# Optimization experiments

Hardware: AMD Instinct MI355X
Metric: run time of the kernel (lower is better)

## Reference

```python
import jax, jax.numpy as jnp
import numpy as np

B, N, C, K, TOPK = 16, 4096, 256, 8, 2
EPS = 1e-6
RATIO = 0.1      # gate_geno_ratio
TEMP = 1.0       # gate_temperature


def setup_inputs() -> dict:
    key = jax.random.key(0)
    ks = jax.random.split(key, 8)
    s = np.float32(1.0 / np.sqrt(C))  # ~xavier scale for C->C linears
    return {
        "tokens": jax.random.normal(ks[0], (B, N, C), jnp.float32),
        "geno_vec": jax.random.normal(ks[1], (B, C), jnp.float32),
        # gate params (gate_proj init std=0.001; gate_geno given small random instead of exact-zero init so it contributes)
        "Wg": jax.random.normal(ks[2], (K, C), jnp.float32) * 0.001,
        "bg": jnp.zeros((K,), jnp.float32),
        "Wgg": jax.random.normal(ks[3], (K, C), jnp.float32) * 0.001,
        "bgg": jnp.zeros((K,), jnp.float32),
        # per-expert 2-layer MLP params (dropout inactive in eval)
        "W1": jax.random.normal(ks[4], (K, C, C), jnp.float32) * s,
        "b1": jnp.zeros((K, C), jnp.float32),
        "W2": jax.random.normal(ks[5], (K, C, C), jnp.float32) * s,
        "b2": jnp.zeros((K, C), jnp.float32),
    }


def reference(tokens, geno_vec, Wg, bg, Wgg, bgg, W1, b1, W2, b2):
    # gate logits: [B,N,K]
    logits = jnp.einsum("bnc,kc->bnk", tokens, Wg) + bg
    logits = logits + RATIO * (geno_vec @ Wgg.T + bgg)[:, None, :]
    logits = logits / TEMP

    topv, topi = jax.lax.top_k(logits, TOPK)          # [B,N,TOPK]
    topw = jax.nn.softmax(topv, axis=-1)
    topw = jnp.maximum(topw, EPS)
    topw = topw / topw.sum(-1, keepdims=True)

    # dense gate weight matrix W: [B,N,K] (scatter of topw at topi; topk indices are distinct)
    hot = jax.nn.one_hot(topi, K, dtype=tokens.dtype)  # [B,N,TOPK,K]
    Wmat = (hot * topw[..., None]).sum(-2)             # [B,N,K]

    # load-balance loss on hard usage (detached in original)
    usage = jax.lax.stop_gradient(hot.sum(-2).mean((0, 1)))  # [K]
    lb_loss = (jnp.std(usage) / (usage.mean() + EPS)) ** 2

    mass_sum = Wmat.sum(axis=1)                        # [B,K]

    # per-expert MLP computed densely over all tokens; zero gate weight kills
    # non-routed tokens exactly (same math as gather->MLP->scatter-add)
    def expert_center(k):
        h = jax.nn.relu(tokens @ W1[k].T + b1[k])      # [B,N,C]
        out = h @ W2[k].T + b2[k]                      # [B,N,C]
        return jnp.einsum("bn,bnc->bc", Wmat[:, :, k], out)

    centers_sum = jnp.stack([expert_center(k) for k in range(K)], axis=1)  # [B,K,C]
    centers = centers_sum / jnp.maximum(mass_sum, EPS)[..., None]

    routing_confidence = (topv[:, :, 0] - topv[:, :, 1]).mean()
    return centers, lb_loss, routing_confidence
```

## Files before the change

### kernel.cpp

```cpp
#include <hip/hip_runtime.h>

#define B_ 16
#define N_ 4096
#define C_ 256
#define K_ 8
#define EPS 1e-6f
#define RATIO 0.1f

typedef float f32x4 __attribute__((ext_vector_type(4)));
typedef __bf16 bf16x8 __attribute__((ext_vector_type(8)));

__device__ inline unsigned short f2bf(float f){
  unsigned int u = __float_as_uint(f);
  u += 0x7FFFu + ((u >> 16) & 1u);
  return (unsigned short)(u >> 16);
}
__device__ inline float bf2f(unsigned short h){
  return __uint_as_float(((unsigned int)h) << 16);
}

union BFu { ushort4 u4[2]; bf16x8 v; };

__global__ __launch_bounds__(256) void k0_prep(
    const float* __restrict__ W1, const float* __restrict__ Wg,
    const float* __restrict__ geno, const float* __restrict__ Wgg,
    const float* __restrict__ bgg,
    unsigned short* __restrict__ W1swz,
    unsigned short* __restrict__ Wgp_hi, unsigned short* __restrict__ Wgp_lo,
    int* __restrict__ cnt,
    float* __restrict__ mass, float* __restrict__ conf,
    float* __restrict__ glog)
{
  int gid = blockIdx.x * 256 + threadIdx.x;
  if (gid < B_*K_) { cnt[gid] = 0; mass[gid] = 0.f; }
  if (gid == 0) conf[0] = 0.f;
  {
    int o = gid << 3;
    int lane6 = (o >> 3) & 63;
    int s  = (o >> 9) & 7;
    int nt = (o >> 12) & 15;
    int k  = o >> 16;
    int quad = lane6 >> 4, l16 = lane6 & 15;
    int j  = nt*16 + l16;
    int c0 = s*32 + quad*8;
    const float* src = W1 + (k << 16) + (j << 8) + c0;
    unsigned short* dst = W1swz + o;
    #pragma unroll
    for (int e = 0; e < 8; ++e) dst[e] = f2bf(src[e]);
  }
  if (gid < 16*C_){
    int r = gid >> 8, c = gid & 255;
    float v = (r < K_) ? Wg[(r << 8) + c] : 0.f;
    unsigned short h = f2bf(v);
    Wgp_hi[gid] = h;
    Wgp_lo[gid] = f2bf(v - bf2f(h));
  }
  int wv = gid >> 6;
  if (wv < B_*K_){
    int lane = threadIdx.x & 63;
    int b = wv >> 3, k = wv & 7;
    float4 a = *(const float4*)(geno + b*C_ + lane*4);
    float4 w = *(const float4*)(Wgg  + k*C_ + lane*4);
    float p = a.x*w.x + a.y*w.y + a.z*w.z + a.w*w.w;
    #pragma unroll
    for (int off = 32; off; off >>= 1) p += __shfl_xor(p, off);
    if (lane == 0) glog[wv] = RATIO * (p + bgg[k]);
  }
}

__global__ __launch_bounds__(256) void k1_gate(
    const float* __restrict__ tokens,
    const unsigned short* __restrict__ Wgp_hi, const unsigned short* __restrict__ Wgp_lo,
    const float* __restrict__ bg, const float* __restrict__ glog,
    int* __restrict__ cnt, int* __restrict__ bidx, float* __restrict__ bw,
    float* __restrict__ mass, float* __restrict__ conf,
    unsigned short* __restrict__ tok_bf)
{
  __shared__ float ls[64][9];
  __shared__ float bg_s[K_], gl_s[K_], mass_s[K_];
  __shared__ int lcnt[K_], gbase[K_];
  __shared__ int e0s[64], e1s[64], s0s[64], s1s[64];
  __shared__ float w0s[64], w1s[64];
  int tid = threadIdx.x, lane = tid & 63, wave = tid >> 6;
  int quad = lane >> 4, l16 = lane & 15;
  int b = blockIdx.x >> 6;
  int tok0 = (blockIdx.x & 63) * 64;
  if (tid < K_){ bg_s[tid] = bg[tid]; gl_s[tid] = glog[b*K_ + tid];
                 mass_s[tid] = 0.f; lcnt[tid] = 0; }
  __syncthreads();

  {
    int trow = tok0 + wave*16 + l16;
    const float* xsrc = tokens + ((size_t)b*N_ + trow)*C_ + quad*8;
    unsigned short* bdst = tok_bf + (((size_t)(b*N_ + trow)) << 8) + quad*8;
    f32x4 acc; acc.x = 0.f; acc.y = 0.f; acc.z = 0.f; acc.w = 0.f;
    #pragma unroll
    for (int s = 0; s < 8; ++s){
      float4 xa = *(const float4*)(xsrc + s*32);
      float4 xb = *(const float4*)(xsrc + s*32 + 4);
      BFu hi, lo;
      hi.u4[0].x = f2bf(xa.x); hi.u4[0].y = f2bf(xa.y);
      hi.u4[0].z = f2bf(xa.z); hi.u4[0].w = f2bf(xa.w);
      hi.u4[1].x = f2bf(xb.x); hi.u4[1].y = f2bf(xb.y);
      hi.u4[1].z = f2bf(xb.z); hi.u4[1].w = f2bf(xb.w);
      lo.u4[0].x = f2bf(xa.x - bf2f(hi.u4[0].x));
      lo.u4[0].y = f2bf(xa.y - bf2f(hi.u4[0].y));
      lo.u4[0].z = f2bf(xa.z - bf2f(hi.u4[0].z));
      lo.u4[0].w = f2bf(xa.w - bf2f(hi.u4[0].w));
      lo.u4[1].x = f2bf(xb.x - bf2f(hi.u4[1].x));
      lo.u4[1].y = f2bf(xb.y - bf2f(hi.u4[1].y));
      lo.u4[1].z = f2bf(xb.z - bf2f(hi.u4[1].z));
      lo.u4[1].w = f2bf(xb.w - bf2f(hi.u4[1].w));
      *(ushort4*)(bdst + s*32)     = hi.u4[0];
      *(ushort4*)(bdst + s*32 + 4) = hi.u4[1];
      bf16x8 bhi = *(const bf16x8*)(Wgp_hi + l16*C_ + s*32 + quad*8);
      bf16x8 blo = *(const bf16x8*)(Wgp_lo + l16*C_ + s*32 + quad*8);
      acc = __builtin_amdgcn_mfma_f32_16x16x32_bf16(hi.v, bhi, acc, 0, 0, 0);
      acc = __builtin_amdgcn_mfma_f32_16x16x32_bf16(lo.v, bhi, acc, 0, 0, 0);
      acc = __builtin_amdgcn_mfma_f32_16x16x32_bf16(hi.v, blo, acc, 0, 0, 0);
    }
    if (l16 < K_){
      #pragma unroll
      for (int rr = 0; rr < 4; ++rr){
        int tl = wave*16 + quad*4 + rr;
        ls[tl][l16] = acc[rr] + bg_s[l16] + gl_s[l16];
      }
    }
  }
  __syncthreads();

  if (tid < 64){
    int t = tid;
    float v0 = -1e30f, v1 = -1e30f; int i0 = 0, i1 = 0;
    #pragma unroll
    for (int kk = 0; kk < K_; ++kk){
      float l = ls[t][kk];
      if (l > v0){ v1 = v0; i1 = i0; v0 = l; i0 = kk; }
      else if (l > v1){ v1 = l; i1 = kk; }
    }
    float e  = expf(v1 - v0);
    float w0 = 1.f / (1.f + e), w1 = e / (1.f + e);
    w0 = fmaxf(w0, EPS); w1 = fmaxf(w1, EPS);
    float inv = 1.f / (w0 + w1);
    w0 *= inv; w1 *= inv;
    int p0 = atomicAdd(&lcnt[i0], 1);
    int p1 = atomicAdd(&lcnt[i1], 1);
    e0s[t] = i0; e1s[t] = i1; s0s[t] = p0; s1s[t] = p1;
    w0s[t] = w0; w1s[t] = w1;
    atomicAdd(&mass_s[i0], w0);
    atomicAdd(&mass_s[i1], w1);
    float ca = v0 - v1;
    #pragma unroll
    for (int off = 32; off; off >>= 1) ca += __shfl_down(ca, off);
    if (t == 0) atomicAdd(conf, ca);
  }
  __syncthreads();
  if (tid < K_){
    gbase[tid] = atomicAdd(&cnt[b*K_ + tid], lcnt[tid]);
    atomicAdd(&mass[b*K_ + tid], mass_s[tid]);
  }
  __syncthreads();
  if (tid < 64){
    int t = tid;
    int n = tok0 + t;
    int ke0 = e0s[t], ke1 = e1s[t];
    size_t o0 = (size_t)(b*K_ + ke0)*N_ + gbase[ke0] + s0s[t];
    size_t o1 = (size_t)(b*K_ + ke1)*N_ + gbase[ke1] + s1s[t];
    bidx[o0] = n;  bw[o0] = w0s[t];
    bidx[o1] = n;  bw[o1] = w1s[t];
  }
}

__global__ void k2_scalars(const int* __restrict__ cnt, const float* __restrict__ conf,
                           float* __restrict__ out)
{
  __shared__ int kc[K_];
  int tid = threadIdx.x;
  if (tid < K_) kc[tid] = 0;
  __syncthreads();
  if (tid < B_*K_) atomicAdd(&kc[tid & 7], cnt[tid]);
  __syncthreads();
  if (tid == 0){
    float u[K_], mean = 0.f;
    for (int k = 0; k < K_; ++k){ u[k] = (float)kc[k] / (float)(B_*N_); mean += u[k]; }
    mean *= (1.f / K_);
    float var = 0.f;
    for (int k = 0; k < K_; ++k){ float d = u[k] - mean; var += d*d; }
    var *= (1.f / K_);
    float denom = mean + EPS;
    out[B_*K_*C_]     = var / (denom * denom);
    out[B_*K_*C_ + 1] = conf[0] / (float)(B_*N_);
  }
}

__global__ __launch_bounds__(256, 4) void k4_expert(
    const unsigned short* __restrict__ tok_bf, const unsigned short* __restrict__ W1swz,
    const float* __restrict__ b1, const int* __restrict__ cnt,
    const int* __restrict__ bidx, const float* __restrict__ bw,
    float* __restrict__ gpart)
{
  int lin = blockIdx.x;
  int w = (lin & 7) * 512 + (lin >> 3);
  int bat = w >> 8;
  int k = (w >> 5) & 7;
  int chunk = w & 31;
  int bucket = (bat << 3) | k;
  int M = cnt[bucket];
  if (chunk * 128 >= M) return;
  int Mm1 = M - 1;

  __shared__ unsigned short Bs[16384];
  __shared__ float wtok[128];
  __shared__ float red[4][64];

  int tid = threadIdx.x, lane = tid & 63, wave = tid >> 6;
  int quad = lane >> 4, l16 = lane & 15;
  int bwbase = bucket << 12;

  const unsigned short* wsrc = W1swz + ((size_t)k << 16);
  #pragma unroll
  for (int i = 0; i < 8; ++i){
    int c16 = i*256 + tid;
    __builtin_amdgcn_global_load_lds(
      (const __attribute__((address_space(1))) unsigned int*)(wsrc + c16*8),
      (__attribute__((address_space(3))) unsigned int*)(Bs + c16*8), 16, 0, 0);
  }

  if (tid < 128){
    int tn = chunk*128 + tid;
    wtok[tid] = (tn < M) ? bw[bwbase + tn] : 0.f;
  }

  int r0 = chunk*128 + (wave << 4) + l16;
  int r1 = r0 + 64;
  int nn0 = bidx[bwbase + min(r0, Mm1)];
  int nn1 = bidx[bwbase + min(r1, Mm1)];
  const unsigned short* p0 = tok_bf + (((size_t)((bat << 12) + nn0)) << 8) + (quad << 3);
  const unsigned short* p1 = tok_bf + (((size_t)((bat << 12) + nn1)) << 8) + (quad << 3);
  bf16x8 a0[8], a1[8];
  #pragma unroll
  for (int s = 0; s < 8; ++s){
    a0[s] = *(const bf16x8*)(p0 + s*32);
    a1[s] = *(const bf16x8*)(p1 + s*32);
  }

  #pragma unroll 1
  for (int jt = 0; jt < 4; ++jt){
    __syncthreads();

    f32x4 acc[2][4];
    #pragma unroll
    for (int mt = 0; mt < 2; ++mt)
      #pragma unroll
      for (int t = 0; t < 4; ++t){ acc[mt][t].x=0.f; acc[mt][t].y=0.f; acc[mt][t].z=0.f; acc[mt][t].w=0.f; }
    #pragma unroll
    for (int s = 0; s < 8; ++s){
      #pragma unroll
      for (int t = 0; t < 4; ++t){
        bf16x8 bb = *(const bf16x8*)(Bs + (((t*8 + s)*64 + lane) << 3));
        acc[0][t] = __builtin_amdgcn_mfma_f32_16x16x32_bf16(a0[s], bb, acc[0][t], 0,0,0);
        acc[1][t] = __builtin_amdgcn_mfma_f32_16x16x32_bf16(a1[s], bb, acc[1][t], 0,0,0);
      }
    }
    #pragma unroll
    for (int t = 0; t < 4; ++t){
      float bias = b1[(k << 8) + (jt << 6) + (t << 4) + l16];
      float pt = 0.f;
      #pragma unroll
      for (int mt = 0; mt < 2; ++mt){
        #pragma unroll
        for (int rr = 0; rr < 4; ++rr){
          float h = fmaxf(acc[mt][t][rr] + bias, 0.f);
          pt += wtok[mt*64 + (wave << 4) + (quad << 2) + rr] * h;
        }
      }
      pt += __shfl_down(pt, 32);
      pt += __shfl_down(pt, 16);
      if (lane < 16) red[wave][(t << 4) + lane] = pt;
    }
    __syncthreads();
    if (tid < 64){
      float sv = red[0][tid] + red[1][tid] + red[2][tid] + red[3][tid];
      gpart[(size_t)((((bucket << 5) + chunk) << 8) + (jt << 6) + tid)] = sv;
    }
    if (jt < 3){
      const unsigned short* ws2 = wsrc + ((jt + 1) << 14);
      #pragma unroll
      for (int i = 0; i < 8; ++i){
        int c16 = i*256 + tid;
        __builtin_amdgcn_global_load_lds(
          (const __attribute__((address_space(1))) unsigned int*)(ws2 + c16*8),
          (__attribute__((address_space(3))) unsigned int*)(Bs + c16*8), 16, 0, 0);
      }
    }
  }
}

__global__ __launch_bounds__(256) void k5_centers(
    const float* __restrict__ gpart, const int* __restrict__ cnt,
    const float* __restrict__ W2, const float* __restrict__ b2,
    const float* __restrict__ mass, float* __restrict__ out)
{
  __shared__ float gv[C_];
  int z = blockIdx.x, tid = threadIdx.x;
  int k = z & 7;
  int nch = (cnt[z] + 127) >> 7;
  float sv = 0.f;
  for (int c = 0; c < nch; ++c)
    sv += gpart[(size_t)((((z << 5) + c) << 8) + tid)];
  gv[tid] = sv;
  __syncthreads();
  float m = mass[z];
  float inv = 1.f / fmaxf(m, EPS);
  int tq = tid & 3, cb = tid >> 2;
  #pragma unroll 1
  for (int h = 0; h < 2; ++h){
    int c = (blockIdx.y*2 + h)*64 + cb;
    const float4* wrow = (const float4*)(W2 + ((((k << 8) + c)) << 8));
    float dot = 0.f;
    #pragma unroll
    for (int jj = 0; jj < 16; ++jj){
      float4 w4 = wrow[jj*4 + tq];
      float4 g4 = *(const float4*)&gv[(jj*4 + tq) * 4];
      dot += w4.x*g4.x + w4.y*g4.y + w4.z*g4.z + w4.w*g4.w;
    }
    dot += __shfl_xor(dot, 1);
    dot += __shfl_xor(dot, 2);
    if (tq == 0) out[z*C_ + c] = (dot + m * b2[k*C_ + c]) * inv;
  }
}

extern "C" void kernel_launch(void* const* d_in, const int* in_sizes, int n_in,
                              void* d_out, int out_size, void* d_ws, size_t ws_size,
                              hipStream_t stream)
{
  const float* tokens = (const float*)d_in[0];
  const float* geno   = (const float*)d_in[1];
  const float* Wg     = (const float*)d_in[2];
  const float* bg     = (const float*)d_in[3];
  const float* Wgg    = (const float*)d_in[4];
  const float* bgg    = (const float*)d_in[5];
  const float* W1     = (const float*)d_in[6];
  const float* b1     = (const float*)d_in[7];
  const float* W2     = (const float*)d_in[8];
  const float* b2     = (const float*)d_in[9];
  float* out = (float*)d_out;
  char* ws = (char*)d_ws;
  unsigned short* W1swz  = (unsigned short*)(ws);
  unsigned short* Wgp_hi = (unsigned short*)(ws + 1048576);
  unsigned short* Wgp_lo = (unsigned short*)(ws + 1056768);
  float* glog = (float*)(ws + 1196032);
  int*   cnt  = (int*)  (ws + 1196544);
  float* mass = (float*)(ws + 1197056);
  float* conf = (float*)(ws + 1197568);
  int*   bidx = (int*)  (ws + 1198080);
  float* bw   = (float*)(ws + 3295232);
  unsigned short* tok_bf = (unsigned short*)(ws + 5392384);
  float* gpart = (float*)(ws + 38946816);

  k0_prep<<<256, 256, 0, stream>>>(W1, Wg, geno, Wgg, bgg, W1swz, Wgp_hi, Wgp_lo,
                                   cnt, mass, conf, glog);
  k1_gate<<<1024, 256, 0, stream>>>(tokens, Wgp_hi, Wgp_lo, bg, glog,
                                    cnt, bidx, bw, mass, conf, tok_bf);
  k2_scalars<<<1, 128, 0, stream>>>(cnt, conf, out);
  k4_expert<<<4096, 256, 0, stream>>>(tok_bf, W1swz, b1, cnt, bidx, bw, gpart);
  k5_centers<<<dim3(128, 2), 256, 0, stream>>>(gpart, cnt, W2, b2, mass, out);
}
```

Measured before the change: 184.0 us.

## Pipeline W1 tiles through a 4-slot LDS ring in expert kernel; fold scalars into k5

```diff
diff --git a/kernel.cpp b/kernel.cpp
--- a/kernel.cpp
+++ b/kernel.cpp
@@ -171,28 +171,6 @@
   }
 }
 
-__global__ void k2_scalars(const int* __restrict__ cnt, const float* __restrict__ conf,
-                           float* __restrict__ out)
-{
-  __shared__ int kc[K_];
-  int tid = threadIdx.x;
-  if (tid < K_) kc[tid] = 0;
-  __syncthreads();
-  if (tid < B_*K_) atomicAdd(&kc[tid & 7], cnt[tid]);
-  __syncthreads();
-  if (tid == 0){
-    float u[K_], mean = 0.f;
-    for (int k = 0; k < K_; ++k){ u[k] = (float)kc[k] / (float)(B_*N_); mean += u[k]; }
-    mean *= (1.f / K_);
-    float var = 0.f;
-    for (int k = 0; k < K_; ++k){ float d = u[k] - mean; var += d*d; }
-    var *= (1.f / K_);
-    float denom = mean + EPS;
-    out[B_*K_*C_]     = var / (denom * denom);
-    out[B_*K_*C_ + 1] = conf[0] / (float)(B_*N_);
-  }
-}
-
 __global__ __launch_bounds__(256, 4) void k4_expert(
     const unsigned short* __restrict__ tok_bf, const unsigned short* __restrict__ W1swz,
     const float* __restrict__ b1, const int* __restrict__ cnt,
@@ -209,21 +187,26 @@
   if (chunk * 128 >= M) return;
   int Mm1 = M - 1;
 
-  __shared__ unsigned short Bs[16384];
+  __shared__ unsigned short Bs[4][4096];
   __shared__ float wtok[128];
-  __shared__ float red[4][64];
+  __shared__ float red[2][4][16];
 
   int tid = threadIdx.x, lane = tid & 63, wave = tid >> 6;
   int quad = lane >> 4, l16 = lane & 15;
   int bwbase = bucket << 12;
 
   const unsigned short* wsrc = W1swz + ((size_t)k << 16);
+
   #pragma unroll
-  for (int i = 0; i < 8; ++i){
-    int c16 = i*256 + tid;
-    __builtin_amdgcn_global_load_lds(
-      (const __attribute__((address_space(1))) unsigned int*)(wsrc + c16*8),
-      (__attribute__((address_space(3))) unsigned int*)(Bs + c16*8), 16, 0, 0);
+  for (int pp = 0; pp < 2; ++pp){
+    #pragma unroll
+    for (int i = 0; i < 2; ++i){
+      int c16 = pp*512 + i*256 + tid;
+      __builtin_amdgcn_global_load_lds(
+        (const __attribute__((address_space(1))) unsigned int*)(wsrc + c16*8),
+        (__attribute__((address_space(3))) unsigned int*)(&Bs[pp][0] + (i*256 + tid)*8),
+        16, 0, 0);
+    }
   }
 
   if (tid < 128){
@@ -232,9 +215,8 @@
   }
 
   int r0 = chunk*128 + (wave << 4) + l16;
-  int r1 = r0 + 64;
   int nn0 = bidx[bwbase + min(r0, Mm1)];
-  int nn1 = bidx[bwbase + min(r1, Mm1)];
+  int nn1 = bidx[bwbase + min(r0 + 64, Mm1)];
   const unsigned short* p0 = tok_bf + (((size_t)((bat << 12) + nn0)) << 8) + (quad << 3);
   const unsigned short* p1 = tok_bf + (((size_t)((bat << 12) + nn1)) << 8) + (quad << 3);
   bf16x8 a0[8], a1[8];
@@ -244,62 +226,72 @@
     a1[s] = *(const bf16x8*)(p1 + s*32);
   }
 
-  #pragma unroll 1
-  for (int jt = 0; jt < 4; ++jt){
-    __syncthreads();
-
-    f32x4 acc[2][4];
-    #pragma unroll
-    for (int mt = 0; mt < 2; ++mt)
+  float bias[16];
+  #pragma unroll
+  for (int p = 0; p < 16; ++p) bias[p] = b1[(k << 8) + (p << 4) + l16];
+
+  float* gdst = gpart + (size_t)(((bucket << 5) + chunk) << 8);
+  int wq = (wave << 4) + (quad << 2);
+
+  #pragma unroll
+  for (int p = 0; p < 16; ++p){
+    if (p < 14){
       #pragma unroll
-      for (int t = 0; t < 4; ++t){ acc[mt][t].x=0.f; acc[mt][t].y=0.f; acc[mt][t].z=0.f; acc[mt][t].w=0.f; }
+      for (int i = 0; i < 2; ++i){
+        int c16 = (p + 2)*512 + i*256 + tid;
+        __builtin_amdgcn_global_load_lds(
+          (const __attribute__((address_space(1))) unsigned int*)(wsrc + c16*8),
+          (__attribute__((address_space(3))) unsigned int*)(&Bs[(p + 2) & 3][0] + (i*256 + tid)*8),
+          16, 0, 0);
+      }
+      asm volatile("s_waitcnt vmcnt(4) lgkmcnt(0)" ::: "memory");
+    } else if (p == 14){
+      asm volatile("s_waitcnt vmcnt(2) lgkmcnt(0)" ::: "memory");
+    } else {
+      asm volatile("s_waitcnt vmcnt(0) lgkmcnt(0)" ::: "memory");
+    }
+    __builtin_amdgcn_s_barrier();
+
+    if (p > 0 && tid < 16){
+      int pb = (p - 1) & 1;
+      float sv = red[pb][0][tid] + red[pb][1][tid]
+               + red[pb][2][tid] + red[pb][3][tid];
+      gdst[((p - 1) << 4) + tid] = sv;
+    }
+
+    f32x4 acc0, acc1;
+    acc0.x=0.f; acc0.y=0.f; acc0.z=0.f; acc0.w=0.f;
+    acc1.x=0.f; acc1.y=0.f; acc1.z=0.f; acc1.w=0.f;
     #pragma unroll
     for (int s = 0; s < 8; ++s){
-      #pragma unroll
-      for (int t = 0; t < 4; ++t){
-        bf16x8 bb = *(const bf16x8*)(Bs + (((t*8 + s)*64 + lane) << 3));
-        acc[0][t] = __builtin_amdgcn_mfma_f32_16x16x32_bf16(a0[s], bb, acc[0][t], 0,0,0);
-        acc[1][t] = __builtin_amdgcn_mfma_f32_16x16x32_bf16(a1[s], bb, acc[1][t], 0,0,0);
-      }
-    }
-    #pragma unroll
-    for (int t = 0; t < 4; ++t){
-      float bias = b1[(k << 8) + (jt << 6) + (t << 4) + l16];
-      float pt = 0.f;
-      #pragma unroll
-      for (int mt = 0; mt < 2; ++mt){
-        #pragma unroll
-        for (int rr = 0; rr < 4; ++rr){
-          float h = fmaxf(acc[mt][t][rr] + bias, 0.f);
-          pt += wtok[mt*64 + (wave << 4) + (quad << 2) + rr] * h;
-        }
-      }
-      pt += __shfl_down(pt, 32);
-      pt += __shfl_down(pt, 16);
-      if (lane < 16) red[wave][(t << 4) + lane] = pt;
-    }
-    __syncthreads();
-    if (tid < 64){
-      float sv = red[0][tid] + red[1][tid] + red[2][tid] + red[3][tid];
-      gpart[(size_t)((((bucket << 5) + chunk) << 8) + (jt << 6) + tid)] = sv;
-    }
-    if (jt < 3){
-      const unsigned short* ws2 = wsrc + ((jt + 1) << 14);
-      #pragma unroll
-      for (int i = 0; i < 8; ++i){
-        int c16 = i*256 + tid;
-        __builtin_amdgcn_global_load_lds(
-          (const __attribute__((address_space(1))) unsigned int*)(ws2 + c16*8),
-          (__attribute__((address_space(3))) unsigned int*)(Bs + c16*8), 16, 0, 0);
-      }
-    }
+      bf16x8 bb = *(const bf16x8*)(&Bs[p & 3][0] + ((s*64 + lane) << 3));
+      acc0 = __builtin_amdgcn_mfma_f32_16x16x32_bf16(a0[s], bb, acc0, 0, 0, 0);
+      acc1 = __builtin_amdgcn_mfma_f32_16x16x32_bf16(a1[s], bb, acc1, 0, 0, 0);
+    }
+    float pt = 0.f;
+    #pragma unroll
+    for (int rr = 0; rr < 4; ++rr){
+      float h0 = fmaxf(acc0[rr] + bias[p], 0.f);
+      float h1 = fmaxf(acc1[rr] + bias[p], 0.f);
+      pt += wtok[wq + rr] * h0 + wtok[64 + wq + rr] * h1;
+    }
+    pt += __shfl_down(pt, 32);
+    pt += __shfl_down(pt, 16);
+    if (lane < 16) red[p & 1][wave][lane] = pt;
+  }
+  asm volatile("s_waitcnt lgkmcnt(0)" ::: "memory");
+  __builtin_amdgcn_s_barrier();
+  if (tid < 16){
+    float sv = red[1][0][tid] + red[1][1][tid] + red[1][2][tid] + red[1][3][tid];
+    gdst[(15 << 4) + tid] = sv;
   }
 }
 
 __global__ __launch_bounds__(256) void k5_centers(
     const float* __restrict__ gpart, const int* __restrict__ cnt,
     const float* __restrict__ W2, const float* __restrict__ b2,
-    const float* __restrict__ mass, float* __restrict__ out)
+    const float* __restrict__ mass, const float* __restrict__ conf,
+    float* __restrict__ out)
 {
   __shared__ float gv[C_];
   int z = blockIdx.x, tid = threadIdx.x;
@@ -327,6 +319,23 @@
     dot += __shfl_xor(dot, 1);
     dot += __shfl_xor(dot, 2);
     if (tq == 0) out[z*C_ + c] = (dot + m * b2[k*C_ + c]) * inv;
+  }
+  if (z == 0 && blockIdx.y == 0 && tid == 0){
+    float u[K_];
+    #pragma unroll
+    for (int kk = 0; kk < K_; ++kk) u[kk] = 0.f;
+    for (int i = 0; i < B_*K_; ++i) u[i & 7] += (float)cnt[i];
+    float mean = 0.f;
+    #pragma unroll
+    for (int kk = 0; kk < K_; ++kk){ u[kk] *= (1.f / (float)(B_*N_)); mean += u[kk]; }
+    mean *= (1.f / K_);
+    float var = 0.f;
+    #pragma unroll
+    for (int kk = 0; kk < K_; ++kk){ float d = u[kk] - mean; var += d*d; }
+    var *= (1.f / K_);
+    float denom = mean + EPS;
+    out[B_*K_*C_]     = var / (denom * denom);
+    out[B_*K_*C_ + 1] = conf[0] / (float)(B_*N_);
   }
 }
 
@@ -362,7 +371,6 @@
                                    cnt, mass, conf, glog);
   k1_gate<<<1024, 256, 0, stream>>>(tokens, Wgp_hi, Wgp_lo, bg, glog,
                                     cnt, bidx, bw, mass, conf, tok_bf);
-  k2_scalars<<<1, 128, 0, stream>>>(cnt, conf, out);
   k4_expert<<<4096, 256, 0, stream>>>(tok_bf, W1swz, b1, cnt, bidx, bw, gpart);
-  k5_centers<<<dim3(128, 2), 256, 0, stream>>>(gpart, cnt, W2, b2, mass, out);
-}
+  k5_centers<<<dim3(128, 2), 256, 0, stream>>>(gpart, cnt, W2, b2, mass, conf, out);
+}
```

Result: faster. 180.1 us (-2.1%).
